# Kernel optimization log

Hardware: AMD Instinct MI355X
Metric: run time of the kernel (lower is better)

The kernel has to match this reference:

```python
import jax, jax.numpy as jnp
import numpy as np

N_HEADS = 16
NEG_INF = -1e30


def setup_inputs() -> dict:
    key = jax.random.key(0)
    ks = jax.random.split(key, 5)
    B, S, D = 2, 2048, 2048
    scale_w = 1.0 / np.sqrt(D)  # keep activations well-scaled
    return {
        "x": jax.random.normal(ks[0], (B, S, D), dtype=jnp.float32),
        "Wq": jax.random.normal(ks[1], (D, D), dtype=jnp.float32) * scale_w,
        "Wk": jax.random.normal(ks[2], (D, D), dtype=jnp.float32) * scale_w,
        "Wv": jax.random.normal(ks[3], (D, D), dtype=jnp.float32) * scale_w,
        "Wo": jax.random.normal(ks[4], (D, D), dtype=jnp.float32) * scale_w,
    }


def reference(x, Wq, Wk, Wv, Wo):
    # Blocked flash attention with online softmax is exactly causal softmax
    # attention; express it directly.
    B, S, D = x.shape
    H = N_HEADS
    dk = D // H
    scale = 1.0 / np.sqrt(dk)

    def heads(w):
        return (x @ w).reshape(B, S, H, dk)

    q = heads(Wq)  # [B,S,H,dk]
    k = heads(Wk)
    v = heads(Wv)

    scores = jnp.einsum("bqhd,bkhd->bhqk", q, k) * scale  # [B,H,S,S]
    causal = jnp.tril(jnp.ones((S, S), dtype=bool))
    scores = jnp.where(causal, scores, NEG_INF)
    p = jax.nn.softmax(scores, axis=-1)
    o = jnp.einsum("bhqk,bkhd->bqhd", p, v).reshape(B, S, D)
    return o @ Wo
```

## Files before the change

kernel.cpp:

```cpp
#include <hip/hip_runtime.h>
#include <hip/hip_bf16.h>

typedef short s16x8 __attribute__((ext_vector_type(8)));
typedef float f32x4 __attribute__((ext_vector_type(4)));
typedef unsigned short u16x4 __attribute__((ext_vector_type(4)));

#define MFMA16(a, b, c) __builtin_amdgcn_mfma_f32_16x16x32_bf16((a), (b), (c), 0, 0, 0)

__device__ __forceinline__ unsigned short f32_to_bf16(float f) {
  unsigned int u = __builtin_bit_cast(unsigned int, f);
  u += 0x7FFFu + ((u >> 16) & 1u);
  return (unsigned short)(u >> 16);
}

__device__ __forceinline__ void glds16(const unsigned short* g, unsigned short* l) {
  __builtin_amdgcn_global_load_lds(
      (const __attribute__((address_space(1))) void*)g,
      (__attribute__((address_space(3))) void*)l, 16, 0, 0);
}

__global__ void cvt_bf16_k(const float* __restrict__ in, unsigned short* __restrict__ out, int n4) {
  int i = blockIdx.x * 256 + threadIdx.x;
  if (i >= n4) return;
  float4 f = ((const float4*)in)[i];
  u16x4 o;
  o.x = f32_to_bf16(f.x); o.y = f32_to_bf16(f.y);
  o.z = f32_to_bf16(f.z); o.w = f32_to_bf16(f.w);
  ((u16x4*)out)[i] = o;
}

__global__ void cvt_t4_k(const float* __restrict__ Wq, const float* __restrict__ Wk,
                         const float* __restrict__ Wv, const float* __restrict__ Wo,
                         unsigned short* __restrict__ outQKV, unsigned short* __restrict__ outO,
                         int D) {
  int z = blockIdx.z;
  const float* in = (z == 0) ? Wq : (z == 1) ? Wk : (z == 2) ? Wv : Wo;
  unsigned short* out = (z < 3) ? (outQKV + (size_t)z * D * D) : outO;
  __shared__ float tile[32][33];
  int tx = threadIdx.x;
  int nt = D >> 5;
  int bx = blockIdx.x % nt;
  int by = blockIdx.x / nt;
  int r = tx >> 3, c4 = (tx & 7) * 4;
  int k0 = by * 32, n0 = bx * 32;
  float4 f = *(const float4*)(in + (size_t)(k0 + r) * D + n0 + c4);
  tile[r][c4 + 0] = f.x; tile[r][c4 + 1] = f.y;
  tile[r][c4 + 2] = f.z; tile[r][c4 + 3] = f.w;
  __syncthreads();
  u16x4 o;
  o.x = f32_to_bf16(tile[c4 + 0][r]);
  o.y = f32_to_bf16(tile[c4 + 1][r]);
  o.z = f32_to_bf16(tile[c4 + 2][r]);
  o.w = f32_to_bf16(tile[c4 + 3][r]);
  *(u16x4*)(out + (size_t)(n0 + r) * D + k0 + c4) = o;
}

template <int OUTF32>
__global__ __launch_bounds__(512, 2) void gemm3(
    const unsigned short* __restrict__ A, const unsigned short* __restrict__ Bt,
    void* __restrict__ Cv, int M, int N, int K, int ldc) {
  __shared__ unsigned short As[3][256 * 64];
  __shared__ unsigned short Bs[3][128 * 64];
  int t = threadIdx.x, lane = t & 63, w = t >> 6;
  int r16 = lane & 15, kg = lane >> 4;
  int wm = w >> 1, wn = w & 1;
  int nbn = N >> 7;
  int bm = blockIdx.x / nbn, bn = blockIdx.x % nbn;
  const unsigned short* Ag = A + (size_t)bm * 256 * K;
  const unsigned short* Bg = Bt + (size_t)bn * 128 * K;

  const unsigned short* asrc[4];
  const unsigned short* bsrc[2];
  int aoff[4], boff[2];
#pragma unroll
  for (int i = 0; i < 4; ++i) {
    int c = i * 512 + t;
    int row = c >> 3, sl = c & 7;
    asrc[i] = Ag + (size_t)row * K + ((sl ^ (row & 7)) * 8);
    aoff[i] = (i * 512 + (t & ~63)) * 8;
  }
#pragma unroll
  for (int i = 0; i < 2; ++i) {
    int c = i * 512 + t;
    int row = c >> 3, sl = c & 7;
    bsrc[i] = Bg + (size_t)row * K + ((sl ^ (row & 7)) * 8);
    boff[i] = (i * 512 + (t & ~63)) * 8;
  }

  auto STAGE = [&](int bi, int kt) {
    int k0 = kt * 64;
#pragma unroll
    for (int i = 0; i < 4; ++i) glds16(asrc[i] + k0, &As[bi][aoff[i]]);
#pragma unroll
    for (int i = 0; i < 2; ++i) glds16(bsrc[i] + k0, &Bs[bi][boff[i]]);
  };

  f32x4 acc[4][4] = {};
  int nt = K >> 6;
  STAGE(0, 0);
  if (nt > 1) STAGE(1, 1);
  int cur = 0;
  for (int kt = 0; kt < nt; ++kt) {
    if (kt + 1 < nt) {
      asm volatile("s_waitcnt vmcnt(6)" ::: "memory");
    } else {
      asm volatile("s_waitcnt vmcnt(0)" ::: "memory");
    }
    __builtin_amdgcn_s_barrier();
    asm volatile("" ::: "memory");
    if (kt + 2 < nt) {
      int s2 = cur + 2; if (s2 >= 3) s2 -= 3;
      STAGE(s2, kt + 2);
    }
    const unsigned short* Al = As[cur];
    const unsigned short* Bl = Bs[cur];
    s16x8 af[4][2], bfr[4][2];
#pragma unroll
    for (int mf = 0; mf < 4; ++mf) {
      int row = wm * 64 + mf * 16 + r16;
#pragma unroll
      for (int ks = 0; ks < 2; ++ks)
        af[mf][ks] = *(const s16x8*)&Al[row * 64 + (((ks * 4 + kg) ^ (row & 7)) * 8)];
    }
#pragma unroll
    for (int nf = 0; nf < 4; ++nf) {
      int row = wn * 64 + nf * 16 + r16;
#pragma unroll
      for (int ks = 0; ks < 2; ++ks)
        bfr[nf][ks] = *(const s16x8*)&Bs[cur][row * 64 + (((ks * 4 + kg) ^ (row & 7)) * 8)];
    }
    (void)Bl;
    __builtin_amdgcn_s_setprio(1);
#pragma unroll
    for (int ks = 0; ks < 2; ++ks)
#pragma unroll
      for (int mf = 0; mf < 4; ++mf)
#pragma unroll
        for (int nf = 0; nf < 4; ++nf)
          acc[mf][nf] = MFMA16(af[mf][ks], bfr[nf][ks], acc[mf][nf]);
    __builtin_amdgcn_s_setprio(0);
    (void)Al;
    cur = (cur == 2) ? 0 : cur + 1;
  }
#pragma unroll
  for (int mf = 0; mf < 4; ++mf)
#pragma unroll
    for (int nf = 0; nf < 4; ++nf)
#pragma unroll
      for (int r = 0; r < 4; ++r) {
        int row = bm * 256 + wm * 64 + mf * 16 + kg * 4 + r;
        int col = bn * 128 + wn * 64 + nf * 16 + r16;
        if (OUTF32)
          ((float*)Cv)[(size_t)row * ldc + col] = acc[mf][nf][r];
        else
          ((unsigned short*)Cv)[(size_t)row * ldc + col] = f32_to_bf16(acc[mf][nf][r]);
      }
}

__global__ __launch_bounds__(256) void vtr_k(const unsigned short* __restrict__ V,
                                             unsigned short* __restrict__ Vt,
                                             int S, int ld) {
  __shared__ unsigned short T[32 * 128];
  int s0 = blockIdx.x * 32, h = blockIdx.y, b = blockIdx.z;
  int H = gridDim.y;
  int t = threadIdx.x;
  const unsigned short* src = V + (size_t)(b * S + s0) * ld + h * 128;
#pragma unroll
  for (int c = 0; c < 2; ++c) {
    int chunk = c * 256 + t;
    int row = chunk >> 4, slot = chunk & 15;
    glds16(src + (size_t)row * ld + slot * 8, &T[(c * 256 + (t & ~63)) * 8]);
  }
  __syncthreads();
  unsigned short* dst = Vt + ((size_t)(b * H + h) * (S >> 3) + (s0 >> 3)) * 1024;
#pragma unroll
  for (int c = 0; c < 2; ++c) {
    int oc = c * 256 + t;
    int sl = oc >> 7, d = oc & 127;
    s16x8 v;
#pragma unroll
    for (int j = 0; j < 8; ++j) v[j] = (short)T[(sl * 8 + j) * 128 + d];
    *(s16x8*)(dst + (size_t)oc * 8) = v;
  }
}

__global__ __launch_bounds__(512) void attn2_k(
    const unsigned short* __restrict__ Q, const unsigned short* __restrict__ Kx,
    const unsigned short* __restrict__ Vt, unsigned short* __restrict__ O,
    int S, int D, int Bn, int ld) {
  const float scale = 0.08838834764831843f;
  int hb = blockIdx.x;
  int h = hb / Bn, b = hb % Bn;
  int qp = blockIdx.y;
  int NQ = S >> 7;
  int H = D >> 7;
  int t = threadIdx.x, lane = t & 63, w = t >> 6;
  int r16 = lane & 15, kg = lane >> 4;
  const unsigned short* Qb  = Q + (size_t)b * S * ld + h * 128;
  const unsigned short* Kb  = Kx + (size_t)b * S * ld + h * 128;
  const unsigned short* Vtb = Vt + (size_t)(b * H + h) * (S >> 3) * 1024;

  __shared__ unsigned short Kbuf[2][64 * 128];
  __shared__ unsigned short Vbuf[2][64 * 128];
  __shared__ unsigned short Pl[8][16 * 64];

  auto STAGE = [&](int bufi, int kv0) {
    const unsigned short* Ksrc = Kb + (size_t)kv0 * ld;
#pragma unroll
    for (int c = 0; c < 2; ++c) {
      int chunk = c * 512 + t;
      int row = chunk >> 4, slot = chunk & 15;
      glds16(Ksrc + (size_t)row * ld + ((slot ^ (row & 7)) * 8),
             &Kbuf[bufi][(c * 512 + (t & ~63)) * 8]);
    }
    const unsigned short* Vsrc = Vtb + (size_t)(kv0 >> 3) * 1024;
#pragma unroll
    for (int c = 0; c < 2; ++c) {
      int chunk = c * 512 + t;
      glds16(Vsrc + (size_t)chunk * 8, &Vbuf[bufi][(c * 512 + (t & ~63)) * 8]);
    }
  };

  for (int hf = 0; hf < 2; ++hf) {
    int qt = hf ? (NQ - 1 - qp) : qp;
    int W0 = qt * 128 + w * 16;
    int qg = W0 + r16;
    s16x8 qf[4];
#pragma unroll
    for (int ks = 0; ks < 4; ++ks)
      qf[ks] = *(const s16x8*)(Qb + (size_t)qg * ld + ks * 32 + kg * 8);
    f32x4 oacc[8] = {};
    float m_st = -1e30f, l_st = 0.f;
    int nt = (qt + 1) * 2;
    int cur = 0;
    STAGE(0, 0);
    __syncthreads();
    for (int it = 0; it < nt; ++it) {
      int kv0 = it * 64;
      if (it + 1 < nt) STAGE(cur ^ 1, (it + 1) * 64);
      const unsigned short* Kl = Kbuf[cur];
      const unsigned short* Vl = Vbuf[cur];
      if (kv0 <= W0 + 15) {
        f32x4 st4[4];
        __builtin_amdgcn_s_setprio(1);
#pragma unroll
        for (int kf = 0; kf < 4; ++kf) {
          f32x4 s = {};
#pragma unroll
          for (int ks = 0; ks < 4; ++ks) {
            int row = kf * 16 + r16;
            s16x8 kfr = *(const s16x8*)&Kl[row * 128 + (((ks * 4 + kg) ^ (row & 7)) * 8)];
            s = MFMA16(kfr, qf[ks], s);
          }
          st4[kf] = s;
        }
        __builtin_amdgcn_s_setprio(0);
        float p[4][4];
        float mx = -1e30f;
#pragma unroll
        for (int kf = 0; kf < 4; ++kf)
#pragma unroll
          for (int r = 0; r < 4; ++r) {
            int kvg = kv0 + kf * 16 + kg * 4 + r;
            float sv = st4[kf][r] * scale;
            sv = (kvg <= qg) ? sv : -1e30f;
            p[kf][r] = sv;
            mx = fmaxf(mx, sv);
          }
        mx = fmaxf(mx, __shfl_xor(mx, 16, 64));
        mx = fmaxf(mx, __shfl_xor(mx, 32, 64));
        float m_new = fmaxf(m_st, mx);
        float alpha = __expf(m_st - m_new);
        float rs = 0.f;
#pragma unroll
        for (int kf = 0; kf < 4; ++kf)
#pragma unroll
          for (int r = 0; r < 4; ++r) {
            float e = __expf(p[kf][r] - m_new);
            p[kf][r] = e;
            rs += e;
          }
        rs += __shfl_xor(rs, 16, 64);
        rs += __shfl_xor(rs, 32, 64);
        l_st = l_st * alpha + rs;
        m_st = m_new;
#pragma unroll
        for (int kf = 0; kf < 4; ++kf) {
          unsigned int lo = (unsigned int)f32_to_bf16(p[kf][0]) | ((unsigned int)f32_to_bf16(p[kf][1]) << 16);
          unsigned int hi = (unsigned int)f32_to_bf16(p[kf][2]) | ((unsigned int)f32_to_bf16(p[kf][3]) << 16);
          int sslot = 2 * kf + (kg >> 1);
          int base = r16 * 64 + ((sslot ^ (r16 & 7)) * 8) + (kg & 1) * 4;
          *(unsigned int*)&Pl[w][base]     = lo;
          *(unsigned int*)&Pl[w][base + 2] = hi;
        }
        asm volatile("s_waitcnt lgkmcnt(0)" ::: "memory");
        __builtin_amdgcn_sched_barrier(0);
        float ar[4];
#pragma unroll
        for (int r = 0; r < 4; ++r) ar[r] = __shfl(alpha, kg * 4 + r, 64);
#pragma unroll
        for (int f = 0; f < 8; ++f)
#pragma unroll
          for (int r = 0; r < 4; ++r) oacc[f][r] *= ar[r];
        __builtin_amdgcn_s_setprio(1);
#pragma unroll
        for (int tt = 0; tt < 2; ++tt) {
          s16x8 pf = *(const s16x8*)&Pl[w][r16 * 64 + (((4 * tt + kg) ^ (r16 & 7)) * 8)];
#pragma unroll
          for (int f = 0; f < 8; ++f) {
            s16x8 vf = *(const s16x8*)&Vl[((4 * tt + kg) * 128 + f * 16 + r16) * 8];
            oacc[f] = MFMA16(pf, vf, oacc[f]);
          }
        }
        __builtin_amdgcn_s_setprio(0);
      }
      __syncthreads();
      cur ^= 1;
    }
    float linv = 1.0f / l_st;
    float lr[4];
#pragma unroll
    for (int r = 0; r < 4; ++r) lr[r] = __shfl(linv, kg * 4 + r, 64);
#pragma unroll
    for (int f = 0; f < 8; ++f)
#pragma unroll
      for (int r = 0; r < 4; ++r) {
        size_t idx = ((size_t)b * S + W0 + kg * 4 + r) * D + h * 128 + f * 16 + r16;
        O[idx] = f32_to_bf16(oacc[f][r] * lr[r]);
      }
  }
}

extern "C" void kernel_launch(void* const* d_in, const int* in_sizes, int n_in,
                              void* d_out, int out_size, void* d_ws, size_t ws_size,
                              hipStream_t stream) {
  const float* x  = (const float*)d_in[0];
  const float* Wq = (const float*)d_in[1];
  const float* Wk = (const float*)d_in[2];
  const float* Wv = (const float*)d_in[3];
  const float* Wo = (const float*)d_in[4];
  const int D = 2048, H = 16;
  const int M = in_sizes[0] / D;
  const int B = 2, S = M / B;
  const int LD = 3 * D;

  unsigned short* xb    = (unsigned short*)d_ws;
  unsigned short* Wqkvt = xb + (size_t)M * D;
  unsigned short* Wot   = Wqkvt + (size_t)3 * D * D;
  unsigned short* QKVb  = Wot + (size_t)D * D;
  unsigned short* Ob    = xb;
  unsigned short* VtA   = Wqkvt;

  int n4 = M * D / 4;
  cvt_bf16_k<<<(n4 + 255) / 256, 256, 0, stream>>>(x, xb, n4);
  int tgrid = (D / 32) * (D / 32);
  cvt_t4_k<<<dim3(tgrid, 1, 4), 256, 0, stream>>>(Wq, Wk, Wv, Wo, Wqkvt, Wot, D);

  gemm3<0><<<(M / 256) * (LD / 128), 512, 0, stream>>>(xb, Wqkvt, QKVb, M, LD, D, LD);

  vtr_k<<<dim3(S / 32, H, B), 256, 0, stream>>>(QKVb + 2 * D, VtA, S, LD);

  attn2_k<<<dim3(H * B, S / 256), 512, 0, stream>>>(QKVb, QKVb + D, VtA, Ob, S, D, B, LD);

  gemm3<1><<<(M / 256) * (D / 128), 512, 0, stream>>>(Ob, Wot, d_out, M, D, D, D);
}
```

Measured before the change: 286.6 us.

## Interleave GEMM LDS reads with MFMA, split global staging, add XCD-aware block swizzle

Block indices are remapped so consecutive tiles land on the same XCD, which should improve L2 reuse of shared A/B panels. The k-loop now loads B fragments once and streams A fragments per m-fragment, running MFMAs immediately. The global-to-LDS prefetch is split into two parts so it overlaps with compute. Extra s_barriers inside the loop add synchronisation cost. The vmcnt(6) wait still assumes six outstanding loads per stage, which holds because the two parts total six.

After: 327.6 us. 14.3% more time.

```diff
diff --git a/kernel.cpp b/kernel.cpp
--- a/kernel.cpp
+++ b/kernel.cpp
@@ -65,7 +65,11 @@
   int r16 = lane & 15, kg = lane >> 4;
   int wm = w >> 1, wn = w & 1;
   int nbn = N >> 7;
-  int bm = blockIdx.x / nbn, bn = blockIdx.x % nbn;
+  int nwg = gridDim.x;
+  int qq = nwg >> 3, rr = nwg & 7;
+  int xcd = blockIdx.x & 7, idx = blockIdx.x >> 3;
+  int swz = (xcd < rr ? xcd * (qq + 1) : rr * (qq + 1) + (xcd - rr) * qq) + idx;
+  int bm = swz / nbn, bn = swz % nbn;
   const unsigned short* Ag = A + (size_t)bm * 256 * K;
   const unsigned short* Bg = Bt + (size_t)bn * 128 * K;
 
@@ -87,18 +91,30 @@
     boff[i] = (i * 512 + (t & ~63)) * 8;
   }
 
-  auto STAGE = [&](int bi, int kt) {
-    int k0 = kt * 64;
+  auto STAGE_ALL = [&](int bi, int kt2) {
+    int k0 = kt2 * 64;
 #pragma unroll
     for (int i = 0; i < 4; ++i) glds16(asrc[i] + k0, &As[bi][aoff[i]]);
 #pragma unroll
     for (int i = 0; i < 2; ++i) glds16(bsrc[i] + k0, &Bs[bi][boff[i]]);
   };
+  auto STAGE_P1 = [&](int bi, int kt2) {
+    int k0 = kt2 * 64;
+    glds16(asrc[0] + k0, &As[bi][aoff[0]]);
+    glds16(asrc[1] + k0, &As[bi][aoff[1]]);
+    glds16(asrc[2] + k0, &As[bi][aoff[2]]);
+  };
+  auto STAGE_P2 = [&](int bi, int kt2) {
+    int k0 = kt2 * 64;
+    glds16(asrc[3] + k0, &As[bi][aoff[3]]);
+    glds16(bsrc[0] + k0, &Bs[bi][boff[0]]);
+    glds16(bsrc[1] + k0, &Bs[bi][boff[1]]);
+  };
 
   f32x4 acc[4][4] = {};
   int nt = K >> 6;
-  STAGE(0, 0);
-  if (nt > 1) STAGE(1, 1);
+  STAGE_ALL(0, 0);
+  if (nt > 1) STAGE_ALL(1, 1);
   int cur = 0;
   for (int kt = 0; kt < nt; ++kt) {
     if (kt + 1 < nt) {
@@ -107,39 +123,36 @@
       asm volatile("s_waitcnt vmcnt(0)" ::: "memory");
     }
     __builtin_amdgcn_s_barrier();
-    asm volatile("" ::: "memory");
-    if (kt + 2 < nt) {
-      int s2 = cur + 2; if (s2 >= 3) s2 -= 3;
-      STAGE(s2, kt + 2);
-    }
+    __builtin_amdgcn_sched_barrier(0);
+    int s2 = cur + 2; if (s2 >= 3) s2 -= 3;
+    if (kt + 2 < nt) STAGE_P1(s2, kt + 2);
     const unsigned short* Al = As[cur];
     const unsigned short* Bl = Bs[cur];
-    s16x8 af[4][2], bfr[4][2];
+    s16x8 bfr[4][2];
+#pragma unroll
+    for (int nf = 0; nf < 4; ++nf) {
+      int row = wn * 64 + nf * 16 + r16;
+#pragma unroll
+      for (int ks = 0; ks < 2; ++ks)
+        bfr[nf][ks] = *(const s16x8*)&Bl[row * 64 + (((ks * 4 + kg) ^ (row & 7)) * 8)];
+    }
 #pragma unroll
     for (int mf = 0; mf < 4; ++mf) {
       int row = wm * 64 + mf * 16 + r16;
-#pragma unroll
-      for (int ks = 0; ks < 2; ++ks)
-        af[mf][ks] = *(const s16x8*)&Al[row * 64 + (((ks * 4 + kg) ^ (row & 7)) * 8)];
-    }
-#pragma unroll
-    for (int nf = 0; nf < 4; ++nf) {
-      int row = wn * 64 + nf * 16 + r16;
-#pragma unroll
-      for (int ks = 0; ks < 2; ++ks)
-        bfr[nf][ks] = *(const s16x8*)&Bs[cur][row * 64 + (((ks * 4 + kg) ^ (row & 7)) * 8)];
-    }
-    (void)Bl;
-    __builtin_amdgcn_s_setprio(1);
-#pragma unroll
-    for (int ks = 0; ks < 2; ++ks)
-#pragma unroll
-      for (int mf = 0; mf < 4; ++mf)
-#pragma unroll
-        for (int nf = 0; nf < 4; ++nf)
-          acc[mf][nf] = MFMA16(af[mf][ks], bfr[nf][ks], acc[mf][nf]);
-    __builtin_amdgcn_s_setprio(0);
-    (void)Al;
+      s16x8 a0 = *(const s16x8*)&Al[row * 64 + ((kg ^ (row & 7)) * 8)];
+      s16x8 a1 = *(const s16x8*)&Al[row * 64 + (((4 + kg) ^ (row & 7)) * 8)];
+      __builtin_amdgcn_s_setprio(1);
+#pragma unroll
+      for (int nf = 0; nf < 4; ++nf) acc[mf][nf] = MFMA16(a0, bfr[nf][0], acc[mf][nf]);
+#pragma unroll
+      for (int nf = 0; nf < 4; ++nf) acc[mf][nf] = MFMA16(a1, bfr[nf][1], acc[mf][nf]);
+      __builtin_amdgcn_s_setprio(0);
+      if (mf == 0 && kt + 2 < nt) STAGE_P2(s2, kt + 2);
+      if (mf < 3) {
+        __builtin_amdgcn_s_barrier();
+        __builtin_amdgcn_sched_barrier(0);
+      }
+    }
     cur = (cur == 2) ? 0 : cur + 1;
   }
 #pragma unroll
```

## Add 256x256-tile GEMM with half-tile interleaved loads for QKV projection

Applied to the files above, without the earlier changes.

Adds a new gemm256 kernel that computes a 256x256 output tile per 512-thread block, with 8 waves arranged 2x4, each computing a 128x64 sub-tile. Global-to-LDS loads are split into half-tiles and interleaved with four MFMA phases separated by barriers, double-buffering A and B. The QKV projection GEMM now uses this kernel, aiming for higher arithmetic intensity and better overlap of loads with MFMA. The cost is more accumulator registers (32 f32x4 per thread), more barriers per K step, and fewer blocks in the grid.

After: 304.1 us. 1.06x slower.

```diff
diff --git a/kernel.cpp b/kernel.cpp
--- a/kernel.cpp
+++ b/kernel.cpp
@@ -18,6 +18,9 @@
       (const __attribute__((address_space(1))) void*)g,
       (__attribute__((address_space(3))) void*)l, 16, 0, 0);
 }
+
+#define BAR() { asm volatile("" ::: "memory"); __builtin_amdgcn_s_barrier(); \
+                __builtin_amdgcn_sched_barrier(0); }
 
 __global__ void cvt_bf16_k(const float* __restrict__ in, unsigned short* __restrict__ out, int n4) {
   int i = blockIdx.x * 256 + threadIdx.x;
@@ -56,6 +59,149 @@
 }
 
 template <int OUTF32>
+__global__ __launch_bounds__(512, 2) void gemm256(
+    const unsigned short* __restrict__ A, const unsigned short* __restrict__ Bt,
+    void* __restrict__ Cv, int M, int N, int K, int ldc) {
+  __shared__ unsigned short Asl[4][128 * 64];
+  __shared__ unsigned short Bsl[4][128 * 64];
+  int t = threadIdx.x, lane = t & 63, w = t >> 6;
+  int r16 = lane & 15, kg = lane >> 4;
+  int wm = w >> 2, wn = w & 3;
+  int nbn = N >> 8;
+  int bm = blockIdx.x / nbn, bn = blockIdx.x % nbn;
+  const unsigned short* Ag = A + (size_t)bm * 256 * K;
+  const unsigned short* Bg = Bt + (size_t)bn * 256 * K;
+
+  const unsigned short* asrc[2][2];
+  const unsigned short* bsrc[2][2];
+  int doff[2];
+#pragma unroll
+  for (int i = 0; i < 2; ++i) {
+    int c = i * 512 + t;
+    int r = c >> 3, s = c & 7;
+    int col = (s ^ (r & 7)) * 8;
+#pragma unroll
+    for (int h = 0; h < 2; ++h) {
+      asrc[h][i] = Ag + (size_t)(h * 128 + r) * K + col;
+      bsrc[h][i] = Bg + (size_t)(h * 128 + r) * K + col;
+    }
+    doff[i] = (i * 512 + (t & ~63)) * 8;
+  }
+
+#define HTA(tt, h) { int sl_ = (((tt) & 1) << 1) + (h); int ko_ = (tt) * 64; \
+    glds16(asrc[h][0] + ko_, &Asl[sl_][doff[0]]); \
+    glds16(asrc[h][1] + ko_, &Asl[sl_][doff[1]]); }
+#define HTB(tt, h) { int sl_ = (((tt) & 1) << 1) + (h); int ko_ = (tt) * 64; \
+    glds16(bsrc[h][0] + ko_, &Bsl[sl_][doff[0]]); \
+    glds16(bsrc[h][1] + ko_, &Bsl[sl_][doff[1]]); }
+
+  f32x4 acc[8][4] = {};
+  int nt = K >> 6;
+  HTA(0, 0); HTA(0, 1); HTB(0, 0); HTB(0, 1); HTA(1, 0); HTA(1, 1);
+  asm volatile("s_waitcnt vmcnt(4)" ::: "memory");
+  __builtin_amdgcn_s_barrier();
+  __builtin_amdgcn_sched_barrier(0);
+
+  for (int kt = 0; kt < nt; ++kt) {
+    int sA = ((kt & 1) << 1) + wm;
+    int sB = ((kt & 1) << 1) + (wn >> 1);
+    int rB0 = (wn & 1) * 64;
+    s16x8 af[8][2], bq[2][2], bq2[2][2];
+    if (kt + 1 < nt) HTB(kt + 1, 0);
+#pragma unroll
+    for (int mf = 0; mf < 4; ++mf) {
+      int rl = mf * 16 + r16;
+#pragma unroll
+      for (int ks = 0; ks < 2; ++ks)
+        af[mf][ks] = *(const s16x8*)&Asl[sA][rl * 64 + (((ks * 4 + kg) ^ (r16 & 7)) * 8)];
+    }
+#pragma unroll
+    for (int nf = 0; nf < 2; ++nf) {
+      int rl = rB0 + nf * 16 + r16;
+#pragma unroll
+      for (int ks = 0; ks < 2; ++ks)
+        bq[nf][ks] = *(const s16x8*)&Bsl[sB][rl * 64 + (((ks * 4 + kg) ^ (r16 & 7)) * 8)];
+    }
+    __builtin_amdgcn_s_setprio(1);
+#pragma unroll
+    for (int ks = 0; ks < 2; ++ks)
+#pragma unroll
+      for (int mf = 0; mf < 4; ++mf)
+#pragma unroll
+        for (int nf = 0; nf < 2; ++nf)
+          acc[mf][nf] = MFMA16(af[mf][ks], bq[nf][ks], acc[mf][nf]);
+    __builtin_amdgcn_s_setprio(0);
+    BAR();
+    if (kt + 1 < nt) HTB(kt + 1, 1);
+#pragma unroll
+    for (int mf = 4; mf < 8; ++mf) {
+      int rl = mf * 16 + r16;
+#pragma unroll
+      for (int ks = 0; ks < 2; ++ks)
+        af[mf][ks] = *(const s16x8*)&Asl[sA][rl * 64 + (((ks * 4 + kg) ^ (r16 & 7)) * 8)];
+    }
+    __builtin_amdgcn_s_setprio(1);
+#pragma unroll
+    for (int ks = 0; ks < 2; ++ks)
+#pragma unroll
+      for (int mf = 4; mf < 8; ++mf)
+#pragma unroll
+        for (int nf = 0; nf < 2; ++nf)
+          acc[mf][nf] = MFMA16(af[mf][ks], bq[nf][ks], acc[mf][nf]);
+    __builtin_amdgcn_s_setprio(0);
+    BAR();
+    if (kt + 2 < nt) HTA(kt + 2, 0);
+#pragma unroll
+    for (int nf = 0; nf < 2; ++nf) {
+      int rl = rB0 + (nf + 2) * 16 + r16;
+#pragma unroll
+      for (int ks = 0; ks < 2; ++ks)
+        bq2[nf][ks] = *(const s16x8*)&Bsl[sB][rl * 64 + (((ks * 4 + kg) ^ (r16 & 7)) * 8)];
+    }
+    __builtin_amdgcn_s_setprio(1);
+#pragma unroll
+    for (int ks = 0; ks < 2; ++ks)
+#pragma unroll
+      for (int mf = 0; mf < 4; ++mf)
+#pragma unroll
+        for (int nf = 0; nf < 2; ++nf)
+          acc[mf][nf + 2] = MFMA16(af[mf][ks], bq2[nf][ks], acc[mf][nf + 2]);
+    __builtin_amdgcn_s_setprio(0);
+    BAR();
+    if (kt + 2 < nt) HTA(kt + 2, 1);
+    __builtin_amdgcn_s_setprio(1);
+#pragma unroll
+    for (int ks = 0; ks < 2; ++ks)
+#pragma unroll
+      for (int mf = 4; mf < 8; ++mf)
+#pragma unroll
+        for (int nf = 0; nf < 2; ++nf)
+          acc[mf][nf + 2] = MFMA16(af[mf][ks], bq2[nf][ks], acc[mf][nf + 2]);
+    __builtin_amdgcn_s_setprio(0);
+    if (kt + 1 < nt) {
+      if (kt + 2 < nt) { asm volatile("s_waitcnt vmcnt(4)" ::: "memory"); }
+      else             { asm volatile("s_waitcnt vmcnt(0)" ::: "memory"); }
+    }
+    BAR();
+  }
+#undef HTA
+#undef HTB
+#pragma unroll
+  for (int mf = 0; mf < 8; ++mf)
+#pragma unroll
+    for (int nf = 0; nf < 4; ++nf)
+#pragma unroll
+      for (int r = 0; r < 4; ++r) {
+        int row = bm * 256 + wm * 128 + mf * 16 + kg * 4 + r;
+        int col = bn * 256 + wn * 64 + nf * 16 + r16;
+        if (OUTF32)
+          ((float*)Cv)[(size_t)row * ldc + col] = acc[mf][nf][r];
+        else
+          ((unsigned short*)Cv)[(size_t)row * ldc + col] = f32_to_bf16(acc[mf][nf][r]);
+      }
+}
+
+template <int OUTF32>
 __global__ __launch_bounds__(512, 2) void gemm3(
     const unsigned short* __restrict__ A, const unsigned short* __restrict__ Bt,
     void* __restrict__ Cv, int M, int N, int K, int ldc) {
@@ -87,8 +233,8 @@
     boff[i] = (i * 512 + (t & ~63)) * 8;
   }
 
-  auto STAGE = [&](int bi, int kt) {
-    int k0 = kt * 64;
+  auto STAGE = [&](int bi, int kt2) {
+    int k0 = kt2 * 64;
 #pragma unroll
     for (int i = 0; i < 4; ++i) glds16(asrc[i] + k0, &As[bi][aoff[i]]);
 #pragma unroll
@@ -113,7 +259,6 @@
       STAGE(s2, kt + 2);
     }
     const unsigned short* Al = As[cur];
-    const unsigned short* Bl = Bs[cur];
     s16x8 af[4][2], bfr[4][2];
 #pragma unroll
     for (int mf = 0; mf < 4; ++mf) {
@@ -129,7 +274,6 @@
       for (int ks = 0; ks < 2; ++ks)
         bfr[nf][ks] = *(const s16x8*)&Bs[cur][row * 64 + (((ks * 4 + kg) ^ (row & 7)) * 8)];
     }
-    (void)Bl;
     __builtin_amdgcn_s_setprio(1);
 #pragma unroll
     for (int ks = 0; ks < 2; ++ks)
@@ -139,7 +283,6 @@
         for (int nf = 0; nf < 4; ++nf)
           acc[mf][nf] = MFMA16(af[mf][ks], bfr[nf][ks], acc[mf][nf]);
     __builtin_amdgcn_s_setprio(0);
-    (void)Al;
     cur = (cur == 2) ? 0 : cur + 1;
   }
 #pragma unroll
@@ -356,7 +499,7 @@
   int tgrid = (D / 32) * (D / 32);
   cvt_t4_k<<<dim3(tgrid, 1, 4), 256, 0, stream>>>(Wq, Wk, Wv, Wo, Wqkvt, Wot, D);
 
-  gemm3<0><<<(M / 256) * (LD / 128), 512, 0, stream>>>(xb, Wqkvt, QKVb, M, LD, D, LD);
+  gemm256<0><<<(M / 256) * (LD / 256), 512, 0, stream>>>(xb, Wqkvt, QKVb, M, LD, D, LD);
 
   vtr_k<<<dim3(S / 32, H, B), 256, 0, stream>>>(QKVb + 2 * D, VtA, S, LD);
 
```
